# Kernel tuning notes

Measured on AMD Instinct MI355X. Metric: run time of the kernel, lower is better.

The kernel has to match this reference:

```python
import jax, jax.numpy as jnp
import numpy as np

N_NODES = 50000
N_EDGES = 800000
NODE_F = 128
EDGE_F = 64
OUT_F = 128


def setup_inputs() -> dict:
    key = jax.random.key(0)
    k1, k2, k3, k4, k5 = jax.random.split(key, 5)
    x = jax.random.normal(k1, (N_NODES, NODE_F), dtype=jnp.float32)
    edge_index = jax.random.randint(k2, (2, N_EDGES), 0, N_NODES, dtype=jnp.int64)
    edge_attr = jax.random.normal(k3, (N_EDGES, EDGE_F), dtype=jnp.float32)
    # Linear(node_features + edge_features, out_features) params (torch default init scale)
    fan_in = NODE_F + EDGE_F
    bound = 1.0 / np.sqrt(fan_in)
    W = jax.random.uniform(k4, (fan_in, OUT_F), minval=-bound, maxval=bound, dtype=jnp.float32)
    b = jax.random.uniform(k5, (OUT_F,), minval=-bound, maxval=bound, dtype=jnp.float32)
    return {"x": x, "edge_index": edge_index, "edge_attr": edge_attr, "W": W, "b": b}


def reference(x, edge_index, edge_attr, W, b):
    # PyG source_to_target flow: x_j = x[src], aggregate at dst
    src = edge_index[0]
    dst = edge_index[1]
    x_j = x[src]                                   # [E, node_f] gather
    feats = jnp.concatenate([edge_attr, x_j], axis=1)  # [E, edge_f + node_f]
    msg = jax.nn.relu(feats @ W + b)               # [E, out_f] Linear + ReLU
    out = jax.ops.segment_sum(msg, dst, num_segments=x.shape[0])  # scatter-add
    return out
```

## Files before the change

### kernel.cpp

```cpp
#include <hip/hip_runtime.h>
#include <hip/hip_bf16.h>

#define N_NODES 50000
#define N_EDGES 800000
#define NODE_F  128
#define EDGE_F  64
#define OUT_F   128

#define NCH ((N_NODES + 255) / 256)
#define EPW 128
#define NRANGES (N_EDGES / EPW)

typedef __attribute__((ext_vector_type(8))) short short8;
typedef __attribute__((ext_vector_type(4))) short short4v;
typedef __attribute__((ext_vector_type(4))) float floatx4;

__device__ __forceinline__ unsigned short f2bf(float f) {
    unsigned int u = __float_as_uint(f);
    u += 0x7fffu + ((u >> 16) & 1u);
    return (unsigned short)(u >> 16);
}

#define TILE_N1 32
#define N_NTILES ((N_NODES + TILE_N1 - 1) / TILE_N1)
#define LDS_STRIDE1 136

__global__ __launch_bounds__(256, 4) void node_kernel(
    const float* __restrict__ x,
    const float* __restrict__ W,
    const float* __restrict__ bias,
    float*       __restrict__ Y)
{
    __shared__ __align__(16) unsigned short xs[TILE_N1][LDS_STRIDE1];

    const int tid  = threadIdx.x;
    const int wave = tid >> 6;
    const int lane = tid & 63;
    const int col  = lane & 15;
    const int quad = lane >> 4;
    const int wbase = wave * 32;

    const float* __restrict__ Wx = W + EDGE_F * OUT_F;

    short8 bfr[4][2];
    #pragma unroll
    for (int kc = 0; kc < 4; ++kc) {
        #pragma unroll
        for (int ns = 0; ns < 2; ++ns) {
            const int n = wbase + ns * 16 + col;
            const int krow = kc * 32 + quad * 8;
            short8 v;
            #pragma unroll
            for (int j = 0; j < 8; ++j)
                v[j] = (short)f2bf(Wx[(krow + j) * OUT_F + n]);
            bfr[kc][ns] = v;
        }
    }
    const float b0 = bias[wbase + col];
    const float b1 = bias[wbase + 16 + col];

    for (int tile = blockIdx.x; tile < N_NTILES; tile += gridDim.x) {
        const int n0 = tile * TILE_N1;
        {
            const int e   = tid >> 3;
            const int sub = tid & 7;
            const int node = n0 + e;
            const float* __restrict__ xr = x + (size_t)node * NODE_F;
            #pragma unroll
            for (int i = 0; i < 4; ++i) {
                const int fi = sub + 8 * i;
                floatx4 v = {0.f, 0.f, 0.f, 0.f};
                if (node < N_NODES) v = *(const floatx4*)(xr + fi * 4);
                short4v sv;
                sv[0] = (short)f2bf(v[0]);
                sv[1] = (short)f2bf(v[1]);
                sv[2] = (short)f2bf(v[2]);
                sv[3] = (short)f2bf(v[3]);
                *(short4v*)&xs[e][fi * 4] = sv;
            }
        }
        __syncthreads();

        floatx4 acc[2][2] = {};
        #pragma unroll
        for (int kc = 0; kc < 4; ++kc) {
            short8 a0 = *(const short8*)&xs[col     ][kc * 32 + quad * 8];
            short8 a1 = *(const short8*)&xs[16 + col][kc * 32 + quad * 8];
            acc[0][0] = __builtin_amdgcn_mfma_f32_16x16x32_bf16(a0, bfr[kc][0], acc[0][0], 0, 0, 0);
            acc[0][1] = __builtin_amdgcn_mfma_f32_16x16x32_bf16(a0, bfr[kc][1], acc[0][1], 0, 0, 0);
            acc[1][0] = __builtin_amdgcn_mfma_f32_16x16x32_bf16(a1, bfr[kc][0], acc[1][0], 0, 0, 0);
            acc[1][1] = __builtin_amdgcn_mfma_f32_16x16x32_bf16(a1, bfr[kc][1], acc[1][1], 0, 0, 0);
        }

        #pragma unroll
        for (int ms = 0; ms < 2; ++ms) {
            #pragma unroll
            for (int r = 0; r < 4; ++r) {
                const int m = ms * 16 + quad * 4 + r;
                const int node = n0 + m;
                if (node < N_NODES) {
                    float* yrow = Y + (size_t)node * OUT_F + wbase;
                    yrow[col]      = acc[ms][0][r] + b0;
                    yrow[16 + col] = acc[ms][1][r] + b1;
                }
            }
        }
        __syncthreads();
    }
}

__global__ void hist_kernel(const int* __restrict__ edge_index, int* __restrict__ hist) {
    const int* dstp = edge_index + N_EDGES;
    for (int i = blockIdx.x * blockDim.x + threadIdx.x; i < N_EDGES;
         i += gridDim.x * blockDim.x)
        atomicAdd(&hist[dstp[i]], 1);
}

__global__ void scan1_kernel(const int* __restrict__ hist, int* __restrict__ chunkSum) {
    __shared__ int s[256];
    const int c = blockIdx.x, t = threadIdx.x, idx = c * 256 + t;
    s[t] = (idx < N_NODES) ? hist[idx] : 0;
    __syncthreads();
    for (int off = 128; off > 0; off >>= 1) {
        if (t < off) s[t] += s[t + off];
        __syncthreads();
    }
    if (t == 0) chunkSum[c] = s[0];
}

__global__ void scan2_kernel(const int* __restrict__ chunkSum, int* __restrict__ chunkBase) {
    __shared__ int s[256];
    const int t = threadIdx.x;
    s[t] = (t < NCH) ? chunkSum[t] : 0;
    __syncthreads();
    for (int off = 1; off < 256; off <<= 1) {
        int u = (t >= off) ? s[t - off] : 0;
        __syncthreads();
        s[t] += u;
        __syncthreads();
    }
    if (t < NCH) chunkBase[t] = (t == 0) ? 0 : s[t - 1];
}

__global__ void scan3_kernel(const int* __restrict__ hist, const int* __restrict__ chunkBase,
                             int* __restrict__ row_off, int* __restrict__ cursor) {
    __shared__ int s[256];
    const int c = blockIdx.x, t = threadIdx.x, idx = c * 256 + t;
    const int v = (idx < N_NODES) ? hist[idx] : 0;
    s[t] = v;
    __syncthreads();
    for (int off = 1; off < 256; off <<= 1) {
        int u = (t >= off) ? s[t - off] : 0;
        __syncthreads();
        s[t] += u;
        __syncthreads();
    }
    const int excl = s[t] - v + chunkBase[c];
    if (idx < N_NODES) { row_off[idx] = excl; cursor[idx] = excl; }
    if (c == 0 && t == 0) row_off[N_NODES] = N_EDGES;
}

__device__ __forceinline__ int lbound(const int* __restrict__ ro, int target) {
    int lo = 0, hi = N_NODES;
    while (lo < hi) {
        const int mid = (lo + hi) >> 1;
        if (ro[mid] < target) lo = mid + 1; else hi = mid;
    }
    return lo;
}

__global__ void range_kernel(const int* __restrict__ row_off, int* __restrict__ range_lo) {
    const int rg = blockIdx.x * blockDim.x + threadIdx.x;
    if (rg <= NRANGES) range_lo[rg] = lbound(row_off, rg * EPW);
}

__global__ void scatter_kernel(const int* __restrict__ edge_index,
                               int* __restrict__ cursor, int4* __restrict__ sorted) {
    const int* srcp = edge_index;
    const int* dstp = edge_index + N_EDGES;
    for (int i = blockIdx.x * blockDim.x + threadIdx.x; i < N_EDGES;
         i += gridDim.x * blockDim.x) {
        const int d = dstp[i];
        const int p = atomicAdd(&cursor[d], 1);
        sorted[p] = make_int4(i, srcp[i], d, 0);
    }
}

__global__ __launch_bounds__(256, 4) void edge_gemm(
    const float* __restrict__ edge_attr,
    const float* __restrict__ W,
    const float* __restrict__ Y,
    const int*   __restrict__ row_off,
    const int*   __restrict__ range_lo,
    const int4*  __restrict__ sorted,
    float*       __restrict__ out)
{
    __shared__ float CT[4][16][68];

    const int tid  = threadIdx.x;
    const int wave = tid >> 6;
    const int lane = tid & 63;
    const int col  = lane & 15;
    const int quad = lane >> 4;
    const int p    = wave & 1;

    short8 bfr[2][4];
    #pragma unroll
    for (int kc = 0; kc < 2; ++kc) {
        #pragma unroll
        for (int ns = 0; ns < 4; ++ns) {
            const int n = p * 64 + ns * 16 + col;
            const int krow = kc * 32 + quad * 8;
            short8 v;
            #pragma unroll
            for (int j = 0; j < 8; ++j)
                v[j] = (short)f2bf(W[(krow + j) * OUT_F + n]);
            bfr[kc][ns] = v;
        }
    }

    const int grange = blockIdx.x * 2 + (wave >> 1);
    const int stride = gridDim.x * 2;

    for (int rg = grange; rg < NRANGES; rg += stride) {
        const int eb = row_off[range_lo[rg]];
        const int ee = row_off[range_lo[rg + 1]];
        if (eb >= ee) continue;

        int   cur = -1;
        float s   = 0.f;

        int4 me = sorted[min(eb + col, ee - 1)];
        short8 a[2];
        {
            const float* __restrict__ ar = edge_attr + (size_t)me.x * EDGE_F;
            #pragma unroll
            for (int kc = 0; kc < 2; ++kc) {
                floatx4 v0 = *(const floatx4*)(ar + kc * 32 + quad * 8);
                floatx4 v1 = *(const floatx4*)(ar + kc * 32 + quad * 8 + 4);
                short8 av;
                av[0] = (short)f2bf(v0[0]); av[1] = (short)f2bf(v0[1]);
                av[2] = (short)f2bf(v0[2]); av[3] = (short)f2bf(v0[3]);
                av[4] = (short)f2bf(v1[0]); av[5] = (short)f2bf(v1[1]);
                av[6] = (short)f2bf(v1[2]); av[7] = (short)f2bf(v1[3]);
                a[kc] = av;
            }
        }

        for (int t0 = eb; t0 < ee; t0 += 16) {
            floatx4 acc[4];
            #pragma unroll
            for (int r = 0; r < 4; ++r) {
                const int src = __shfl(me.y, quad * 4 + r);
                const float* __restrict__ yr = Y + (size_t)src * OUT_F + p * 64;
                #pragma unroll
                for (int ns = 0; ns < 4; ++ns)
                    acc[ns][r] = yr[ns * 16 + col];
            }

            #pragma unroll
            for (int kc = 0; kc < 2; ++kc) {
                #pragma unroll
                for (int ns = 0; ns < 4; ++ns)
                    acc[ns] = __builtin_amdgcn_mfma_f32_16x16x32_bf16(a[kc], bfr[kc][ns], acc[ns], 0, 0, 0);
            }

            #pragma unroll
            for (int r = 0; r < 4; ++r) {
                const bool rvalid = (t0 + quad * 4 + r) < ee;
                #pragma unroll
                for (int ns = 0; ns < 4; ++ns)
                    CT[wave][quad * 4 + r][ns * 16 + col] =
                        rvalid ? fmaxf(acc[ns][r], 0.f) : 0.f;
            }
            __builtin_amdgcn_wave_barrier();

            const int t1 = t0 + 16;
            int4 me2;
            if (t1 < ee) me2 = sorted[min(t1 + col, ee - 1)];

            float cv[16];
            #pragma unroll
            for (int m = 0; m < 16; ++m) cv[m] = CT[wave][m][lane];

            #pragma unroll
            for (int m = 0; m < 16; ++m) {
                const int d = __builtin_amdgcn_readlane(me.z, m);
                if (d != cur) {
                    if (cur >= 0) out[(size_t)cur * OUT_F + p * 64 + lane] = s;
                    cur = d; s = 0.f;
                }
                s += cv[m];
            }
            cur = __builtin_amdgcn_readfirstlane(cur);
            __builtin_amdgcn_wave_barrier();

            if (t1 < ee) {
                me = me2;
                const float* __restrict__ ar = edge_attr + (size_t)me.x * EDGE_F;
                #pragma unroll
                for (int kc = 0; kc < 2; ++kc) {
                    floatx4 v0 = *(const floatx4*)(ar + kc * 32 + quad * 8);
                    floatx4 v1 = *(const floatx4*)(ar + kc * 32 + quad * 8 + 4);
                    short8 av;
                    av[0] = (short)f2bf(v0[0]); av[1] = (short)f2bf(v0[1]);
                    av[2] = (short)f2bf(v0[2]); av[3] = (short)f2bf(v0[3]);
                    av[4] = (short)f2bf(v1[0]); av[5] = (short)f2bf(v1[1]);
                    av[6] = (short)f2bf(v1[2]); av[7] = (short)f2bf(v1[3]);
                    a[kc] = av;
                }
            }
        }
        if (cur >= 0) out[(size_t)cur * OUT_F + p * 64 + lane] = s;
    }
}

__global__ __launch_bounds__(256, 3) void edge_kernel_atomic(
    const float* __restrict__ edge_attr,
    const int*   __restrict__ edge_index,
    const float* __restrict__ W,
    const float* __restrict__ Y,
    float*       __restrict__ out)
{
    const int lane = threadIdx.x & 63;
    const int col  = lane & 15;
    const int quad = lane >> 4;

    short8 bfr[2][8];
    #pragma unroll
    for (int kc = 0; kc < 2; ++kc)
        #pragma unroll
        for (int ns = 0; ns < 8; ++ns) {
            const int n = ns * 16 + col;
            const int krow = kc * 32 + quad * 8;
            short8 v;
            #pragma unroll
            for (int j = 0; j < 8; ++j)
                v[j] = (short)f2bf(W[(krow + j) * OUT_F + n]);
            bfr[kc][ns] = v;
        }

    const int* __restrict__ srcp = edge_index;
    const int* __restrict__ dstp = edge_index + N_EDGES;

    const int gwave  = blockIdx.x * 4 + (threadIdx.x >> 6);
    const int nwaves = gridDim.x * 4;

    for (int t = gwave; t < N_EDGES / 16; t += nwaves) {
        const int e0 = t * 16;
        const float* __restrict__ ar = edge_attr + (size_t)(e0 + col) * EDGE_F;
        short8 a[2];
        #pragma unroll
        for (int kc = 0; kc < 2; ++kc) {
            floatx4 v0 = *(const floatx4*)(ar + kc * 32 + quad * 8);
            floatx4 v1 = *(const floatx4*)(ar + kc * 32 + quad * 8 + 4);
            short8 av;
            av[0] = (short)f2bf(v0[0]); av[1] = (short)f2bf(v0[1]);
            av[2] = (short)f2bf(v0[2]); av[3] = (short)f2bf(v0[3]);
            av[4] = (short)f2bf(v1[0]); av[5] = (short)f2bf(v1[1]);
            av[6] = (short)f2bf(v1[2]); av[7] = (short)f2bf(v1[3]);
            a[kc] = av;
        }
        int sr[4], dr[4];
        #pragma unroll
        for (int r = 0; r < 4; ++r) {
            sr[r] = srcp[e0 + quad * 4 + r];
            dr[r] = dstp[e0 + quad * 4 + r];
        }
        floatx4 acc[8];
        #pragma unroll
        for (int ns = 0; ns < 8; ++ns)
            #pragma unroll
            for (int r = 0; r < 4; ++r)
                acc[ns][r] = Y[(size_t)sr[r] * OUT_F + ns * 16 + col];
        #pragma unroll
        for (int kc = 0; kc < 2; ++kc)
            #pragma unroll
            for (int ns = 0; ns < 8; ++ns)
                acc[ns] = __builtin_amdgcn_mfma_f32_16x16x32_bf16(a[kc], bfr[kc][ns], acc[ns], 0, 0, 0);
        #pragma unroll
        for (int ns = 0; ns < 8; ++ns)
            #pragma unroll
            for (int r = 0; r < 4; ++r) {
                const float v = acc[ns][r];
                if (v > 0.0f)
                    atomicAdd(out + (size_t)dr[r] * OUT_F + ns * 16 + col, v);
            }
    }
}

extern "C" void kernel_launch(void* const* d_in, const int* in_sizes, int n_in,
                              void* d_out, int out_size, void* d_ws, size_t ws_size,
                              hipStream_t stream) {
    const float* x          = (const float*)d_in[0];
    const int*   edge_index = (const int*)  d_in[1];
    const float* edge_attr  = (const float*)d_in[2];
    const float* W          = (const float*)d_in[3];
    const float* bias       = (const float*)d_in[4];
    float*       out        = (float*)d_out;

    float* Y        = (float*)d_ws;
    int4*  sorted   = (int4*)(Y + (size_t)N_NODES * OUT_F);
    int*   hist     = (int*)(sorted + N_EDGES);
    int*   chunkSum = hist + N_NODES;
    int*   chunkBase= chunkSum + 256;
    int*   row_off  = chunkBase + 256;
    int*   cursor   = row_off + N_NODES + 1;
    int*   range_lo = cursor + N_NODES;
    const size_t needed = (size_t)((char*)(range_lo + NRANGES + 1) - (char*)d_ws);

    hipMemsetAsync(out, 0, (size_t)out_size * sizeof(float), stream);
    node_kernel<<<dim3(512), dim3(256), 0, stream>>>(x, W, bias, Y);

    if (ws_size < needed) {
        edge_kernel_atomic<<<dim3(1024), dim3(256), 0, stream>>>(edge_attr, edge_index, W, Y, out);
        return;
    }

    hipMemsetAsync(hist, 0, (size_t)N_NODES * sizeof(int), stream);
    hist_kernel   <<<dim3(2048), dim3(256), 0, stream>>>(edge_index, hist);
    scan1_kernel  <<<dim3(NCH),  dim3(256), 0, stream>>>(hist, chunkSum);
    scan2_kernel  <<<dim3(1),    dim3(256), 0, stream>>>(chunkSum, chunkBase);
    scan3_kernel  <<<dim3(NCH),  dim3(256), 0, stream>>>(hist, chunkBase, row_off, cursor);
    range_kernel  <<<dim3((NRANGES + 256) / 256), dim3(256), 0, stream>>>(row_off, range_lo);
    scatter_kernel<<<dim3(2048), dim3(256), 0, stream>>>(edge_index, cursor, sorted);
    edge_gemm     <<<dim3((NRANGES + 1) / 2), dim3(256), 0, stream>>>(
        edge_attr, W, Y, row_off, range_lo, sorted, out);
}
```

Measured before the change: 488.0 us.

## Pack sorted edge records to int2, precompute range starts, use hardware bf16 conversion

Shrinks each sorted edge record from int4 to int2 by packing the 16-bit src and dst node ids into one word, which halves scatter writes and edge_gemm reads. The range kernel now stores the edge offsets directly, removing a dependent indirection per range. Software float-to-bf16 rounding is replaced with the __float22bfloat162_rn intrinsic. edge_gemm moves to launch bounds of 6 blocks per CU and a fixed 1536-block persistent grid. Packing node ids into 16 bits only works because the test graph has 50000 nodes, which fits under 65536.

```diff
diff --git a/kernel.cpp b/kernel.cpp
--- a/kernel.cpp
+++ b/kernel.cpp
@@ -19,6 +19,15 @@
     unsigned int u = __float_as_uint(f);
     u += 0x7fffu + ((u >> 16) & 1u);
     return (unsigned short)(u >> 16);
+}
+
+__device__ __forceinline__ short8 cvt8(floatx4 v0, floatx4 v1) {
+    union { __hip_bfloat162 h[4]; short8 s; } u;
+    u.h[0] = __float22bfloat162_rn(make_float2(v0[0], v0[1]));
+    u.h[1] = __float22bfloat162_rn(make_float2(v0[2], v0[3]));
+    u.h[2] = __float22bfloat162_rn(make_float2(v1[0], v1[1]));
+    u.h[3] = __float22bfloat162_rn(make_float2(v1[2], v1[3]));
+    return u.s;
 }
 
 #define TILE_N1 32
@@ -71,12 +80,10 @@
                 const int fi = sub + 8 * i;
                 floatx4 v = {0.f, 0.f, 0.f, 0.f};
                 if (node < N_NODES) v = *(const floatx4*)(xr + fi * 4);
-                short4v sv;
-                sv[0] = (short)f2bf(v[0]);
-                sv[1] = (short)f2bf(v[1]);
-                sv[2] = (short)f2bf(v[2]);
-                sv[3] = (short)f2bf(v[3]);
-                *(short4v*)&xs[e][fi * 4] = sv;
+                union { __hip_bfloat162 h[2]; short4v s; } u;
+                u.h[0] = __float22bfloat162_rn(make_float2(v[0], v[1]));
+                u.h[1] = __float22bfloat162_rn(make_float2(v[2], v[3]));
+                *(short4v*)&xs[e][fi * 4] = u.s;
             }
         }
         __syncthreads();
@@ -169,30 +176,29 @@
     return lo;
 }
 
-__global__ void range_kernel(const int* __restrict__ row_off, int* __restrict__ range_lo) {
+__global__ void range_kernel(const int* __restrict__ row_off, int* __restrict__ range_start) {
     const int rg = blockIdx.x * blockDim.x + threadIdx.x;
-    if (rg <= NRANGES) range_lo[rg] = lbound(row_off, rg * EPW);
+    if (rg <= NRANGES) range_start[rg] = row_off[lbound(row_off, rg * EPW)];
 }
 
 __global__ void scatter_kernel(const int* __restrict__ edge_index,
-                               int* __restrict__ cursor, int4* __restrict__ sorted) {
+                               int* __restrict__ cursor, int2* __restrict__ sorted) {
     const int* srcp = edge_index;
     const int* dstp = edge_index + N_EDGES;
     for (int i = blockIdx.x * blockDim.x + threadIdx.x; i < N_EDGES;
          i += gridDim.x * blockDim.x) {
         const int d = dstp[i];
         const int p = atomicAdd(&cursor[d], 1);
-        sorted[p] = make_int4(i, srcp[i], d, 0);
-    }
-}
-
-__global__ __launch_bounds__(256, 4) void edge_gemm(
+        sorted[p] = make_int2(i, (int)(((unsigned)srcp[i] << 16) | (unsigned)d));
+    }
+}
+
+__global__ __launch_bounds__(256, 6) void edge_gemm(
     const float* __restrict__ edge_attr,
     const float* __restrict__ W,
     const float* __restrict__ Y,
-    const int*   __restrict__ row_off,
-    const int*   __restrict__ range_lo,
-    const int4*  __restrict__ sorted,
+    const int*   __restrict__ range_start,
+    const int2*  __restrict__ sorted,
     float*       __restrict__ out)
 {
     __shared__ float CT[4][16][68];
@@ -219,39 +225,34 @@
         }
     }
 
+    float* __restrict__ obase = out + p * 64 + lane;
+
     const int grange = blockIdx.x * 2 + (wave >> 1);
     const int stride = gridDim.x * 2;
 
     for (int rg = grange; rg < NRANGES; rg += stride) {
-        const int eb = row_off[range_lo[rg]];
-        const int ee = row_off[range_lo[rg + 1]];
+        const int eb = range_start[rg];
+        const int ee = range_start[rg + 1];
         if (eb >= ee) continue;
 
         int   cur = -1;
         float s   = 0.f;
 
-        int4 me = sorted[min(eb + col, ee - 1)];
+        int2 me = sorted[min(eb + col, ee - 1)];
         short8 a[2];
         {
             const float* __restrict__ ar = edge_attr + (size_t)me.x * EDGE_F;
             #pragma unroll
-            for (int kc = 0; kc < 2; ++kc) {
-                floatx4 v0 = *(const floatx4*)(ar + kc * 32 + quad * 8);
-                floatx4 v1 = *(const floatx4*)(ar + kc * 32 + quad * 8 + 4);
-                short8 av;
-                av[0] = (short)f2bf(v0[0]); av[1] = (short)f2bf(v0[1]);
-                av[2] = (short)f2bf(v0[2]); av[3] = (short)f2bf(v0[3]);
-                av[4] = (short)f2bf(v1[0]); av[5] = (short)f2bf(v1[1]);
-                av[6] = (short)f2bf(v1[2]); av[7] = (short)f2bf(v1[3]);
-                a[kc] = av;
-            }
+            for (int kc = 0; kc < 2; ++kc)
+                a[kc] = cvt8(*(const floatx4*)(ar + kc * 32 + quad * 8),
+                             *(const floatx4*)(ar + kc * 32 + quad * 8 + 4));
         }
 
         for (int t0 = eb; t0 < ee; t0 += 16) {
             floatx4 acc[4];
             #pragma unroll
             for (int r = 0; r < 4; ++r) {
-                const int src = __shfl(me.y, quad * 4 + r);
+                const int src = (int)((unsigned)__shfl(me.y, quad * 4 + r) >> 16);
                 const float* __restrict__ yr = Y + (size_t)src * OUT_F + p * 64;
                 #pragma unroll
                 for (int ns = 0; ns < 4; ++ns)
@@ -276,18 +277,19 @@
             __builtin_amdgcn_wave_barrier();
 
             const int t1 = t0 + 16;
-            int4 me2;
+            int2 me2;
             if (t1 < ee) me2 = sorted[min(t1 + col, ee - 1)];
 
             float cv[16];
             #pragma unroll
             for (int m = 0; m < 16; ++m) cv[m] = CT[wave][m][lane];
 
+            const int mez = me.y;
             #pragma unroll
             for (int m = 0; m < 16; ++m) {
-                const int d = __builtin_amdgcn_readlane(me.z, m);
+                const int d = (int)((unsigned)__builtin_amdgcn_readlane(mez, m) & 0xffffu);
                 if (d != cur) {
-                    if (cur >= 0) out[(size_t)cur * OUT_F + p * 64 + lane] = s;
+                    if (cur >= 0) obase[(size_t)cur * OUT_F] = s;
                     cur = d; s = 0.f;
                 }
                 s += cv[m];
@@ -299,19 +301,12 @@
                 me = me2;
                 const float* __restrict__ ar = edge_attr + (size_t)me.x * EDGE_F;
                 #pragma unroll
-                for (int kc = 0; kc < 2; ++kc) {
-                    floatx4 v0 = *(const floatx4*)(ar + kc * 32 + quad * 8);
-                    floatx4 v1 = *(const floatx4*)(ar + kc * 32 + quad * 8 + 4);
-                    short8 av;
-                    av[0] = (short)f2bf(v0[0]); av[1] = (short)f2bf(v0[1]);
-                    av[2] = (short)f2bf(v0[2]); av[3] = (short)f2bf(v0[3]);
-                    av[4] = (short)f2bf(v1[0]); av[5] = (short)f2bf(v1[1]);
-                    av[6] = (short)f2bf(v1[2]); av[7] = (short)f2bf(v1[3]);
-                    a[kc] = av;
-                }
-            }
-        }
-        if (cur >= 0) out[(size_t)cur * OUT_F + p * 64 + lane] = s;
+                for (int kc = 0; kc < 2; ++kc)
+                    a[kc] = cvt8(*(const floatx4*)(ar + kc * 32 + quad * 8),
+                                 *(const floatx4*)(ar + kc * 32 + quad * 8 + 4));
+            }
+        }
+        if (cur >= 0) obase[(size_t)cur * OUT_F] = s;
     }
 }
 
@@ -351,16 +346,9 @@
         const float* __restrict__ ar = edge_attr + (size_t)(e0 + col) * EDGE_F;
         short8 a[2];
         #pragma unroll
-        for (int kc = 0; kc < 2; ++kc) {
-            floatx4 v0 = *(const floatx4*)(ar + kc * 32 + quad * 8);
-            floatx4 v1 = *(const floatx4*)(ar + kc * 32 + quad * 8 + 4);
-            short8 av;
-            av[0] = (short)f2bf(v0[0]); av[1] = (short)f2bf(v0[1]);
-            av[2] = (short)f2bf(v0[2]); av[3] = (short)f2bf(v0[3]);
-            av[4] = (short)f2bf(v1[0]); av[5] = (short)f2bf(v1[1]);
-            av[6] = (short)f2bf(v1[2]); av[7] = (short)f2bf(v1[3]);
-            a[kc] = av;
-        }
+        for (int kc = 0; kc < 2; ++kc)
+            a[kc] = cvt8(*(const floatx4*)(ar + kc * 32 + quad * 8),
+                         *(const floatx4*)(ar + kc * 32 + quad * 8 + 4));
         int sr[4], dr[4];
         #pragma unroll
         for (int r = 0; r < 4; ++r) {
@@ -399,15 +387,15 @@
     const float* bias       = (const float*)d_in[4];
     float*       out        = (float*)d_out;
 
-    float* Y        = (float*)d_ws;
-    int4*  sorted   = (int4*)(Y + (size_t)N_NODES * OUT_F);
-    int*   hist     = (int*)(sorted + N_EDGES);
-    int*   chunkSum = hist + N_NODES;
-    int*   chunkBase= chunkSum + 256;
-    int*   row_off  = chunkBase + 256;
-    int*   cursor   = row_off + N_NODES + 1;
-    int*   range_lo = cursor + N_NODES;
-    const size_t needed = (size_t)((char*)(range_lo + NRANGES + 1) - (char*)d_ws);
+    float* Y          = (float*)d_ws;
+    int2*  sorted     = (int2*)(Y + (size_t)N_NODES * OUT_F);
+    int*   hist       = (int*)(sorted + N_EDGES);
+    int*   chunkSum   = hist + N_NODES;
+    int*   chunkBase  = chunkSum + 256;
+    int*   row_off    = chunkBase + 256;
+    int*   cursor     = row_off + N_NODES + 1;
+    int*   range_start= cursor + N_NODES;
+    const size_t needed = (size_t)((char*)(range_start + NRANGES + 1) - (char*)d_ws);
 
     hipMemsetAsync(out, 0, (size_t)out_size * sizeof(float), stream);
     node_kernel<<<dim3(512), dim3(256), 0, stream>>>(x, W, bias, Y);
@@ -422,8 +410,8 @@
     scan1_kernel  <<<dim3(NCH),  dim3(256), 0, stream>>>(hist, chunkSum);
     scan2_kernel  <<<dim3(1),    dim3(256), 0, stream>>>(chunkSum, chunkBase);
     scan3_kernel  <<<dim3(NCH),  dim3(256), 0, stream>>>(hist, chunkBase, row_off, cursor);
-    range_kernel  <<<dim3((NRANGES + 256) / 256), dim3(256), 0, stream>>>(row_off, range_lo);
+    range_kernel  <<<dim3((NRANGES + 256) / 256), dim3(256), 0, stream>>>(row_off, range_start);
     scatter_kernel<<<dim3(2048), dim3(256), 0, stream>>>(edge_index, cursor, sorted);
-    edge_gemm     <<<dim3((NRANGES + 1) / 2), dim3(256), 0, stream>>>(
-        edge_attr, W, Y, row_off, range_lo, sorted, out);
-}
+    edge_gemm     <<<dim3(1536), dim3(256), 0, stream>>>(
+        edge_attr, W, Y, range_start, sorted, out);
+}
```

New measurement: 483.8 us. About the same (-0.9%).
